# Kernel tuning notes

Measured on AMD Instinct MI355X. Metric: run time of the kernel, lower is better.

The kernel has to match this reference:

```python
import jax, jax.numpy as jnp
import numpy as np

HIDDEN = 1024
HEADS = 16
HEAD_DIM = HIDDEN // HEADS
B, S = 2, 2048


def setup_inputs() -> dict:
    key = jax.random.key(0)
    ks = jax.random.split(key, 9)
    sc = 1.0 / np.sqrt(HIDDEN)
    return {
        "hidden_state": jax.random.normal(ks[0], (B, S, HIDDEN), dtype=jnp.float32),
        "wq": jax.random.normal(ks[1], (HIDDEN, HIDDEN), dtype=jnp.float32) * sc,
        "bq": jax.random.normal(ks[2], (HIDDEN,), dtype=jnp.float32) * 0.01,
        "wk": jax.random.normal(ks[3], (HIDDEN, HIDDEN), dtype=jnp.float32) * sc,
        "bk": jax.random.normal(ks[4], (HIDDEN,), dtype=jnp.float32) * 0.01,
        "wv": jax.random.normal(ks[5], (HIDDEN, HIDDEN), dtype=jnp.float32) * sc,
        "bv": jax.random.normal(ks[6], (HIDDEN,), dtype=jnp.float32) * 0.01,
        "wo": jax.random.normal(ks[7], (HIDDEN, HIDDEN), dtype=jnp.float32) * sc,
        "bo": jax.random.normal(ks[8], (HIDDEN,), dtype=jnp.float32) * 0.01,
    }


def reference(hidden_state, wq, bq, wk, bk, wv, bv, wo, bo):
    b, s, _ = hidden_state.shape

    def split_head(x):  # [B,S,H*D] -> [B,H,S,D]
        return x.reshape(b, s, HEADS, HEAD_DIM).transpose(0, 2, 1, 3)

    q = split_head(hidden_state @ wq + bq)
    k = split_head(hidden_state @ wk + bk)
    v = split_head(hidden_state @ wv + bv)

    # NOTE: original scales by sqrt(hidden_size), NOT sqrt(head_dim)
    scale = 1.0 / jnp.sqrt(jnp.float32(HIDDEN))
    scores = jnp.einsum("bhqd,bhkd->bhqk", q, k) * scale  # [B,H,S,S]
    probs = jax.nn.softmax(scores, axis=-1)
    out = jnp.einsum("bhqk,bhkd->bhqd", probs, v)  # [B,H,S,D]

    # Faithful to source: transpose(-1,-2) then view (this is the original's
    # layout, which differs from the conventional transpose(1,2) merge)
    out = out.transpose(0, 1, 3, 2).reshape(b, -1, HEADS * HEAD_DIM)
    return out @ wo + bo
```

## Files before the change

### kernel.cpp

```cpp
#include <hip/hip_runtime.h>
#include <stdint.h>


typedef unsigned short u16;
typedef __bf16 bf16x8 __attribute__((ext_vector_type(8)));
typedef u16 u16x8 __attribute__((ext_vector_type(8)));
typedef u16 u16x4 __attribute__((ext_vector_type(4)));
typedef float f32x4 __attribute__((ext_vector_type(4)));

#define DEV static __device__ __forceinline__

DEV bf16x8 as_bf16x8(u16x8 u) { union { u16x8 u; bf16x8 b; } c; c.u = u; return c.b; }
DEV u16 f2bf(float f) {
  uint32_t u = __float_as_uint(f);
  u += 0x7fffu + ((u >> 16) & 1u);
  return (u16)(u >> 16);
}
#if __has_builtin(__builtin_amdgcn_exp2f)
DEV float ex2(float x) { return __builtin_amdgcn_exp2f(x); }
#else
DEV float ex2(float x) { return exp2f(x); }
#endif

__global__ __launch_bounds__(256) void prep_kernel(
    const float* __restrict__ hid, const float* __restrict__ w0,
    const float* __restrict__ w1, const float* __restrict__ w2,
    const float* __restrict__ w3, u16* __restrict__ Ah,
    u16* __restrict__ Wt) {
  __shared__ __align__(16) float T[64][68];
  int bid = blockIdx.x, t = threadIdx.x;
  if (bid < 2048) {
    int i = (bid * 256 + t) * 8;
    f32x4 a = *(const f32x4*)&hid[i];
    f32x4 b = *(const f32x4*)&hid[i + 4];
    u16x8 o;
#pragma unroll
    for (int j = 0; j < 4; ++j) { o[j] = f2bf(a[j]); o[j + 4] = f2bf(b[j]); }
    *(u16x8*)&Ah[i] = o;
    return;
  }
  int tb = bid - 2048;
  int z = tb >> 8, rem = tb & 255;
  const float* W = (z == 0) ? w0 : (z == 1) ? w1 : (z == 2) ? w2 : w3;
  u16* O = Wt + (size_t)z * 1024 * 1024;
  int r0 = (rem >> 4) * 64, c0 = (rem & 15) * 64;
  int i = t >> 2, js = (t & 3) * 16;
#pragma unroll
  for (int jj = 0; jj < 16; jj += 4)
    *(f32x4*)&T[i][js + jj] = *(const f32x4*)&W[(size_t)(r0 + i) * 1024 + c0 + js + jj];
  __syncthreads();
#pragma unroll
  for (int seg = 0; seg < 2; ++seg) {
    u16x8 v;
#pragma unroll
    for (int jj = 0; jj < 8; ++jj) v[jj] = f2bf(T[js + seg * 8 + jj][i]);
    *(u16x8*)&O[(size_t)(c0 + i) * 1024 + r0 + js + seg * 8] = v;
  }
}

__global__ __launch_bounds__(256, 2) void qkv_gemm(
    const u16* __restrict__ A, const u16* __restrict__ Wt,
    const float* __restrict__ bq, const float* __restrict__ bk,
    const float* __restrict__ bv, u16* __restrict__ Qb, u16* __restrict__ Kb,
    u16* __restrict__ Vt) {
  __shared__ __align__(16) u16 As[2][128 * 32], Bs[2][3][64 * 32];
  int tid = threadIdx.x, lane = tid & 63, w = tid >> 6;
  int quad = lane >> 4, l15 = lane & 15;
  int m0 = blockIdx.x * 128, n0 = blockIdx.y * 64;
  int wm = w >> 1, wn = w & 1;
  f32x4 acc[3][4][2] = {};

  const int idx0 = tid, idx1 = 256 + tid;
  const int arow0 = idx0 >> 2, ac0 = ((idx0 & 3) ^ ((arow0 >> 1) & 3)) * 8;
  const int arow1 = idx1 >> 2, ac1 = ((idx1 & 3) ^ ((arow1 >> 1) & 3)) * 8;
  const u16* Ap0 = A + (size_t)(m0 + arow0) * 1024 + ac0;
  const u16* Ap1 = A + (size_t)(m0 + arow1) * 1024 + ac1;
  const int brow = tid >> 2, bcg = ((tid & 3) ^ ((brow >> 1) & 3)) * 8;
  const u16* Bp0 = Wt + (size_t)(n0 + brow) * 1024 + bcg;
  const u16* Bp1 = Bp0 + (size_t)1024 * 1024;
  const u16* Bp2 = Bp0 + (size_t)2 * 1024 * 1024;

  u16x8 ta0, ta1, tb0, tb1, tb2;
  ta0 = *(const u16x8*)Ap0;
  ta1 = *(const u16x8*)Ap1;
  tb0 = *(const u16x8*)Bp0;
  tb1 = *(const u16x8*)Bp1;
  tb2 = *(const u16x8*)Bp2;
  *(u16x8*)&As[0][idx0 * 8] = ta0;
  *(u16x8*)&As[0][idx1 * 8] = ta1;
  *(u16x8*)&Bs[0][0][tid * 8] = tb0;
  *(u16x8*)&Bs[0][1][tid * 8] = tb1;
  *(u16x8*)&Bs[0][2][tid * 8] = tb2;
  __syncthreads();

  for (int k0 = 0; k0 < 1024; k0 += 32) {
    int cur = (k0 >> 5) & 1;
    if (k0 < 992) {
      ta0 = *(const u16x8*)(Ap0 + k0 + 32);
      ta1 = *(const u16x8*)(Ap1 + k0 + 32);
      tb0 = *(const u16x8*)(Bp0 + k0 + 32);
      tb1 = *(const u16x8*)(Bp1 + k0 + 32);
      tb2 = *(const u16x8*)(Bp2 + k0 + 32);
    }

    bf16x8 af[4];
#pragma unroll
    for (int mt = 0; mt < 4; ++mt) {
      int row = wm * 64 + mt * 16 + l15;
      af[mt] = as_bf16x8(*(const u16x8*)&As[cur][row * 32 + (quad ^ ((row >> 1) & 3)) * 8]);
    }
    __builtin_amdgcn_s_setprio(1);
#pragma unroll
    for (int z = 0; z < 3; ++z) {
      bf16x8 bfr[2];
#pragma unroll
      for (int nt = 0; nt < 2; ++nt) {
        int row = wn * 32 + nt * 16 + l15;
        bfr[nt] = as_bf16x8(*(const u16x8*)&Bs[cur][z][row * 32 + (quad ^ ((row >> 1) & 3)) * 8]);
      }
#pragma unroll
      for (int mt = 0; mt < 4; ++mt)
#pragma unroll
        for (int nt = 0; nt < 2; ++nt)
          acc[z][mt][nt] = __builtin_amdgcn_mfma_f32_16x16x32_bf16(af[mt], bfr[nt], acc[z][mt][nt], 0, 0, 0);
    }
    __builtin_amdgcn_s_setprio(0);

    if (k0 < 992) {
      int nb = cur ^ 1;
      *(u16x8*)&As[nb][idx0 * 8] = ta0;
      *(u16x8*)&As[nb][idx1 * 8] = ta1;
      *(u16x8*)&Bs[nb][0][tid * 8] = tb0;
      *(u16x8*)&Bs[nb][1][tid * 8] = tb1;
      *(u16x8*)&Bs[nb][2][tid * 8] = tb2;
    }
    __syncthreads();
  }

#pragma unroll
  for (int z = 0; z < 2; ++z) {
    const float* bias = (z == 0) ? bq : bk;
    u16* C = (z == 0) ? Qb : Kb;
    float scale = (z == 0) ? 0.045084220f : 1.0f;
#pragma unroll
    for (int nt = 0; nt < 2; ++nt) {
      int n = n0 + wn * 32 + nt * 16 + l15;
      float bb = bias[n];
      int h = n >> 6, d = n & 63;
#pragma unroll
      for (int mt = 0; mt < 4; ++mt) {
        int mbase = m0 + wm * 64 + mt * 16 + quad * 4;
#pragma unroll
        for (int r = 0; r < 4; ++r) {
          int m = mbase + r;
          int b = m >> 11, s = m & 2047;
          C[(((size_t)(b * 16 + h)) * 2048 + s) * 64 + d] =
              f2bf((acc[z][mt][nt][r] + bb) * scale);
        }
      }
    }
  }
#pragma unroll
  for (int nt = 0; nt < 2; ++nt) {
    int n = n0 + wn * 32 + nt * 16 + l15;
    float bb = bv[n];
    int h = n >> 6, d = n & 63;
#pragma unroll
    for (int mt = 0; mt < 4; ++mt) {
      int mbase = m0 + wm * 64 + mt * 16 + quad * 4;
      int b = mbase >> 11, s = mbase & 2047;
      size_t base = (((size_t)(b * 16 + h)) * 64 + d) * 2048 + s;
      u16x4 pk;
#pragma unroll
      for (int r = 0; r < 4; ++r) pk[r] = f2bf(acc[2][mt][nt][r] + bb);
      *(u16x4*)&Vt[base] = pk;
    }
  }
}

__global__ __launch_bounds__(256) void out_gemm(
    const u16* __restrict__ A, const u16* __restrict__ Wt,
    const float* __restrict__ bo, float* __restrict__ C) {
  const u16* Bt = Wt + (size_t)3 * 1024 * 1024;
  __shared__ __align__(16) u16 As[2][64 * 32], Bs[2][128 * 32];
  int tid = threadIdx.x, lane = tid & 63, w = tid >> 6;
  int quad = lane >> 4, l15 = lane & 15;
  int m0 = blockIdx.x * 64, n0 = blockIdx.y * 128;
  f32x4 acc[4][2] = {};

  const int arow = tid >> 2, acg = ((tid & 3) ^ ((arow >> 1) & 3)) * 8;
  const int bidx0 = tid, bidx1 = 256 + tid;
  const int brow0 = bidx0 >> 2, bc0 = ((bidx0 & 3) ^ ((brow0 >> 1) & 3)) * 8;
  const int brow1 = bidx1 >> 2, bc1 = ((bidx1 & 3) ^ ((brow1 >> 1) & 3)) * 8;
  const u16* Ap = A + (size_t)(m0 + arow) * 1024 + acg;
  const u16* Bp0 = Bt + (size_t)(n0 + brow0) * 1024 + bc0;
  const u16* Bp1 = Bt + (size_t)(n0 + brow1) * 1024 + bc1;

  u16x8 ta, tb0, tb1;
  ta = *(const u16x8*)Ap;
  tb0 = *(const u16x8*)Bp0;
  tb1 = *(const u16x8*)Bp1;
  *(u16x8*)&As[0][tid * 8] = ta;
  *(u16x8*)&Bs[0][bidx0 * 8] = tb0;
  *(u16x8*)&Bs[0][bidx1 * 8] = tb1;
  __syncthreads();

  for (int k0 = 0; k0 < 1024; k0 += 32) {
    int cur = (k0 >> 5) & 1;
    if (k0 < 992) {
      ta = *(const u16x8*)(Ap + k0 + 32);
      tb0 = *(const u16x8*)(Bp0 + k0 + 32);
      tb1 = *(const u16x8*)(Bp1 + k0 + 32);
    }

    bf16x8 af[4], bfr[2];
#pragma unroll
    for (int mt = 0; mt < 4; ++mt) {
      int row = mt * 16 + l15;
      af[mt] = as_bf16x8(*(const u16x8*)&As[cur][row * 32 + (quad ^ ((row >> 1) & 3)) * 8]);
    }
#pragma unroll
    for (int nt = 0; nt < 2; ++nt) {
      int row = w * 32 + nt * 16 + l15;
      bfr[nt] = as_bf16x8(*(const u16x8*)&Bs[cur][row * 32 + (quad ^ ((row >> 1) & 3)) * 8]);
    }
    __builtin_amdgcn_s_setprio(1);
#pragma unroll
    for (int mt = 0; mt < 4; ++mt)
#pragma unroll
      for (int nt = 0; nt < 2; ++nt)
        acc[mt][nt] = __builtin_amdgcn_mfma_f32_16x16x32_bf16(af[mt], bfr[nt], acc[mt][nt], 0, 0, 0);
    __builtin_amdgcn_s_setprio(0);

    if (k0 < 992) {
      int nb = cur ^ 1;
      *(u16x8*)&As[nb][tid * 8] = ta;
      *(u16x8*)&Bs[nb][bidx0 * 8] = tb0;
      *(u16x8*)&Bs[nb][bidx1 * 8] = tb1;
    }
    __syncthreads();
  }

#pragma unroll
  for (int nt = 0; nt < 2; ++nt) {
    int n = n0 + w * 32 + nt * 16 + l15;
    float bv = bo[n];
#pragma unroll
    for (int mt = 0; mt < 4; ++mt) {
      int mbase = m0 + mt * 16 + quad * 4;
#pragma unroll
      for (int r = 0; r < 4; ++r)
        C[(size_t)(mbase + r) * 1024 + n] = acc[mt][nt][r] + bv;
    }
  }
}

#define PSTR 80
__global__ __launch_bounds__(256, 2) void attn_kernel(
    const u16* __restrict__ Qb, const u16* __restrict__ Kb,
    const u16* __restrict__ Vtb, u16* __restrict__ Otb) {
  __shared__ __align__(16) u16 Ks[2][64 * PSTR], Vs[2][64 * PSTR];
  int tid = threadIdx.x, lane = tid & 63, w = tid >> 6;
  int quad = lane >> 4, l15 = lane & 15;
  int bh = blockIdx.x, q0 = blockIdx.y * 128;
  const size_t baseQK = (size_t)bh * 2048 * 64;

  bf16x8 bq[2][2];
#pragma unroll
  for (int g = 0; g < 2; ++g) {
    int qrow = q0 + w * 32 + g * 16 + l15;
#pragma unroll
    for (int ks = 0; ks < 2; ++ks)
      bq[g][ks] = as_bf16x8(*(const u16x8*)&Qb[baseQK + (size_t)qrow * 64 + (ks * 4 + quad) * 8]);
  }

  bf16x8 av1;
  {
    u16x8 o1;
#pragma unroll
    for (int j = 0; j < 8; ++j) o1[j] = 0x3F80;
    av1 = as_bf16x8(o1);
  }

  f32x4 o[2][4] = {};
  f32x4 l_acc[2] = {};
  const int km = ((l15 & 12) << 1) | (l15 & 3);
  const int srow = tid >> 3, scs = tid & 7;
  const int srow2 = 32 + srow;

  u16x8 tk[2], tv[2];
  tk[0] = *(const u16x8*)&Kb[baseQK + (size_t)srow * 64 + scs * 8];
  tk[1] = *(const u16x8*)&Kb[baseQK + (size_t)srow2 * 64 + scs * 8];
  tv[0] = *(const u16x8*)&Vtb[baseQK + (size_t)srow * 2048 + scs * 8];
  tv[1] = *(const u16x8*)&Vtb[baseQK + (size_t)srow2 * 2048 + scs * 8];
  *(u16x8*)&Ks[0][srow * PSTR + scs * 8] = tk[0];
  *(u16x8*)&Ks[0][srow2 * PSTR + scs * 8] = tk[1];
  *(u16x8*)&Vs[0][srow * PSTR + scs * 8] = tv[0];
  *(u16x8*)&Vs[0][srow2 * PSTR + scs * 8] = tv[1];
  __syncthreads();

  for (int kv = 0; kv < 32; ++kv) {
    int cur = kv & 1;
    if (kv < 31) {
      tk[0] = *(const u16x8*)&Kb[baseQK + (size_t)((kv + 1) * 64 + srow) * 64 + scs * 8];
      tk[1] = *(const u16x8*)&Kb[baseQK + (size_t)((kv + 1) * 64 + srow2) * 64 + scs * 8];
      tv[0] = *(const u16x8*)&Vtb[baseQK + (size_t)srow * 2048 + (kv + 1) * 64 + scs * 8];
      tv[1] = *(const u16x8*)&Vtb[baseQK + (size_t)srow2 * 2048 + (kv + 1) * 64 + scs * 8];
    }

    f32x4 scA[2][2] = {}, scB[2][2] = {};
    __builtin_amdgcn_s_setprio(1);
#pragma unroll
    for (int ks = 0; ks < 2; ++ks)
#pragma unroll
      for (int mtg = 0; mtg < 2; ++mtg) {
        bf16x8 akA = as_bf16x8(*(const u16x8*)&Ks[cur][(mtg * 32 + km) * PSTR + (ks * 4 + quad) * 8]);
        bf16x8 akB = as_bf16x8(*(const u16x8*)&Ks[cur][(mtg * 32 + km + 4) * PSTR + (ks * 4 + quad) * 8]);
#pragma unroll
        for (int g = 0; g < 2; ++g) {
          scA[g][mtg] = __builtin_amdgcn_mfma_f32_16x16x32_bf16(akA, bq[g][ks], scA[g][mtg], 0, 0, 0);
          scB[g][mtg] = __builtin_amdgcn_mfma_f32_16x16x32_bf16(akB, bq[g][ks], scB[g][mtg], 0, 0, 0);
        }
      }
    __builtin_amdgcn_s_setprio(0);

    bf16x8 bp[2][2];
#pragma unroll
    for (int g = 0; g < 2; ++g)
#pragma unroll
      for (int mtg = 0; mtg < 2; ++mtg) {
        float pA0 = ex2(scA[g][mtg][0]), pA1 = ex2(scA[g][mtg][1]);
        float pA2 = ex2(scA[g][mtg][2]), pA3 = ex2(scA[g][mtg][3]);
        float pB0 = ex2(scB[g][mtg][0]), pB1 = ex2(scB[g][mtg][1]);
        float pB2 = ex2(scB[g][mtg][2]), pB3 = ex2(scB[g][mtg][3]);
        bp[g][mtg] = (bf16x8){(__bf16)pA0, (__bf16)pA1, (__bf16)pA2, (__bf16)pA3,
                              (__bf16)pB0, (__bf16)pB1, (__bf16)pB2, (__bf16)pB3};
        l_acc[g] = __builtin_amdgcn_mfma_f32_16x16x32_bf16(av1, bp[g][mtg], l_acc[g], 0, 0, 0);
      }

    __builtin_amdgcn_s_setprio(1);
#pragma unroll
    for (int mtg = 0; mtg < 2; ++mtg)
#pragma unroll
      for (int dt = 0; dt < 4; ++dt) {
        bf16x8 av = as_bf16x8(*(const u16x8*)&Vs[cur][(dt * 16 + l15) * PSTR + (mtg * 4 + quad) * 8]);
#pragma unroll
        for (int g = 0; g < 2; ++g)
          o[g][dt] = __builtin_amdgcn_mfma_f32_16x16x32_bf16(av, bp[g][mtg], o[g][dt], 0, 0, 0);
      }
    __builtin_amdgcn_s_setprio(0);

    if (kv < 31) {
      int nb = cur ^ 1;
      *(u16x8*)&Ks[nb][srow * PSTR + scs * 8] = tk[0];
      *(u16x8*)&Ks[nb][srow2 * PSTR + scs * 8] = tk[1];
      *(u16x8*)&Vs[nb][srow * PSTR + scs * 8] = tv[0];
      *(u16x8*)&Vs[nb][srow2 * PSTR + scs * 8] = tv[1];
    }
    __syncthreads();
  }

#pragma unroll
  for (int g = 0; g < 2; ++g) {
    float inv = 1.0f / l_acc[g][0];
#pragma unroll
    for (int dt = 0; dt < 4; ++dt)
#pragma unroll
      for (int r = 0; r < 4; ++r) {
        int d = dt * 16 + quad * 4 + r;
        Otb[(size_t)bh * 64 * 2048 + (size_t)d * 2048 + q0 + w * 32 + g * 16 + l15] =
            f2bf(o[g][dt][r] * inv);
      }
  }
}

extern "C" void kernel_launch(void* const* d_in, const int* in_sizes, int n_in,
                              void* d_out, int out_size, void* d_ws, size_t ws_size,
                              hipStream_t stream) {
  const float* hid = (const float*)d_in[0];
  const float* wq = (const float*)d_in[1];
  const float* bq = (const float*)d_in[2];
  const float* wk = (const float*)d_in[3];
  const float* bk = (const float*)d_in[4];
  const float* wv = (const float*)d_in[5];
  const float* bv = (const float*)d_in[6];
  const float* wo = (const float*)d_in[7];
  const float* bo = (const float*)d_in[8];

  u16* ws = (u16*)d_ws;
  const size_t MB2 = (size_t)1024 * 1024;
  u16* Wt  = ws;
  u16* Ah  = ws + 4 * MB2;
  u16* Qb  = ws + 8 * MB2;
  u16* Kb  = ws + 12 * MB2;
  u16* Vtb = ws + 16 * MB2;
  u16* Otb = Ah;

  prep_kernel<<<3072, 256, 0, stream>>>(hid, wq, wk, wv, wo, Ah, Wt);
  qkv_gemm<<<dim3(32, 16), 256, 0, stream>>>(Ah, Wt, bq, bk, bv, Qb, Kb, Vtb);
  attn_kernel<<<dim3(32, 16), 256, 0, stream>>>(Qb, Kb, Vtb, Otb);
  out_gemm<<<dim3(64, 8), 256, 0, stream>>>(Otb, Wt, bo, (float*)d_out);
}
```

Before: 178.6 us.

## Split attention KV range across waves with LDS reduction of partial outputs

The attention kernel now gives each block 64 queries instead of 128 and launches twice as many blocks. Each of the four waves processes a different 32-key slice of a 128-key tile, rather than splitting queries across waves. Because softmax uses no max subtraction, the per-wave partial outputs and denominators can simply be summed with LDS atomics and then normalized. Output stores also become vectorized 16-byte writes. The intent is more parallelism and better occupancy, traded against a single-buffered tile with two barriers per iteration and an atomic reduction epilogue.

```diff
diff --git a/kernel.cpp b/kernel.cpp
--- a/kernel.cpp
+++ b/kernel.cpp
@@ -255,24 +255,30 @@
   }
 }
 
-#define PSTR 80
+#define KSTR 80
+#define VSTR 144
 __global__ __launch_bounds__(256, 2) void attn_kernel(
     const u16* __restrict__ Qb, const u16* __restrict__ Kb,
     const u16* __restrict__ Vtb, u16* __restrict__ Otb) {
-  __shared__ __align__(16) u16 Ks[2][64 * PSTR], Vs[2][64 * PSTR];
+  __shared__ __align__(16) u16 Ks[128 * KSTR];
+  __shared__ __align__(16) u16 Vs[64 * VSTR];
+  __shared__ __align__(16) float Or[64][66];
+  __shared__ float Lr[64];
   int tid = threadIdx.x, lane = tid & 63, w = tid >> 6;
   int quad = lane >> 4, l15 = lane & 15;
-  int bh = blockIdx.x, q0 = blockIdx.y * 128;
+  int bh = blockIdx.x, q0 = blockIdx.y * 64;
   const size_t baseQK = (size_t)bh * 2048 * 64;
 
-  bf16x8 bq[2][2];
-#pragma unroll
-  for (int g = 0; g < 2; ++g) {
-    int qrow = q0 + w * 32 + g * 16 + l15;
+  for (int i = tid; i < 64 * 66; i += 256) (&Or[0][0])[i] = 0.0f;
+  if (tid < 64) Lr[tid] = 0.0f;
+
+  bf16x8 bq[4][2];
+#pragma unroll
+  for (int qt = 0; qt < 4; ++qt)
 #pragma unroll
     for (int ks = 0; ks < 2; ++ks)
-      bq[g][ks] = as_bf16x8(*(const u16x8*)&Qb[baseQK + (size_t)qrow * 64 + (ks * 4 + quad) * 8]);
-  }
+      bq[qt][ks] = as_bf16x8(*(const u16x8*)&Qb[baseQK +
+          (size_t)(q0 + qt * 16 + l15) * 64 + (ks * 4 + quad) * 8]);
 
   bf16x8 av1;
   {
@@ -282,95 +288,99 @@
     av1 = as_bf16x8(o1);
   }
 
-  f32x4 o[2][4] = {};
-  f32x4 l_acc[2] = {};
+  f32x4 o[4][4] = {};
+  f32x4 l_acc[4] = {};
   const int km = ((l15 & 12) << 1) | (l15 & 3);
-  const int srow = tid >> 3, scs = tid & 7;
-  const int srow2 = 32 + srow;
-
-  u16x8 tk[2], tv[2];
-  tk[0] = *(const u16x8*)&Kb[baseQK + (size_t)srow * 64 + scs * 8];
-  tk[1] = *(const u16x8*)&Kb[baseQK + (size_t)srow2 * 64 + scs * 8];
-  tv[0] = *(const u16x8*)&Vtb[baseQK + (size_t)srow * 2048 + scs * 8];
-  tv[1] = *(const u16x8*)&Vtb[baseQK + (size_t)srow2 * 2048 + scs * 8];
-  *(u16x8*)&Ks[0][srow * PSTR + scs * 8] = tk[0];
-  *(u16x8*)&Ks[0][srow2 * PSTR + scs * 8] = tk[1];
-  *(u16x8*)&Vs[0][srow * PSTR + scs * 8] = tv[0];
-  *(u16x8*)&Vs[0][srow2 * PSTR + scs * 8] = tv[1];
+  const int kw = w * 32;
+
+  u16x8 tk[4], tv[4];
+#pragma unroll
+  for (int i = 0; i < 4; ++i) {
+    int ki = i * 256 + tid, kr = ki >> 3, kc = ki & 7;
+    tk[i] = *(const u16x8*)&Kb[baseQK + (size_t)kr * 64 + kc * 8];
+    int vd = ki >> 4, vc = ki & 15;
+    tv[i] = *(const u16x8*)&Vtb[baseQK + (size_t)vd * 2048 + vc * 8];
+  }
+
+  for (int it = 0; it < 16; ++it) {
+    __syncthreads();
+#pragma unroll
+    for (int i = 0; i < 4; ++i) {
+      int ki = i * 256 + tid, kr = ki >> 3, kc = ki & 7;
+      *(u16x8*)&Ks[kr * KSTR + kc * 8] = tk[i];
+      int vd = ki >> 4, vc = ki & 15;
+      *(u16x8*)&Vs[vd * VSTR + vc * 8] = tv[i];
+    }
+    __syncthreads();
+
+    if (it < 15) {
+#pragma unroll
+      for (int i = 0; i < 4; ++i) {
+        int ki = i * 256 + tid, kr = ki >> 3, kc = ki & 7;
+        tk[i] = *(const u16x8*)&Kb[baseQK + (size_t)((it + 1) * 128 + kr) * 64 + kc * 8];
+        int vd = ki >> 4, vc = ki & 15;
+        tv[i] = *(const u16x8*)&Vtb[baseQK + (size_t)vd * 2048 + (it + 1) * 128 + vc * 8];
+      }
+    }
+
+    bf16x8 akA[2], akB[2], av[4];
+#pragma unroll
+    for (int ks = 0; ks < 2; ++ks) {
+      akA[ks] = as_bf16x8(*(const u16x8*)&Ks[(kw + km) * KSTR + (ks * 4 + quad) * 8]);
+      akB[ks] = as_bf16x8(*(const u16x8*)&Ks[(kw + km + 4) * KSTR + (ks * 4 + quad) * 8]);
+    }
+#pragma unroll
+    for (int dt = 0; dt < 4; ++dt)
+      av[dt] = as_bf16x8(*(const u16x8*)&Vs[(dt * 16 + l15) * VSTR + kw + quad * 8]);
+
+#pragma unroll
+    for (int qt = 0; qt < 4; ++qt) {
+      f32x4 sA = {}, sB = {};
+      __builtin_amdgcn_s_setprio(1);
+      sA = __builtin_amdgcn_mfma_f32_16x16x32_bf16(akA[0], bq[qt][0], sA, 0, 0, 0);
+      sA = __builtin_amdgcn_mfma_f32_16x16x32_bf16(akA[1], bq[qt][1], sA, 0, 0, 0);
+      sB = __builtin_amdgcn_mfma_f32_16x16x32_bf16(akB[0], bq[qt][0], sB, 0, 0, 0);
+      sB = __builtin_amdgcn_mfma_f32_16x16x32_bf16(akB[1], bq[qt][1], sB, 0, 0, 0);
+      __builtin_amdgcn_s_setprio(0);
+      float pA0 = ex2(sA[0]), pA1 = ex2(sA[1]), pA2 = ex2(sA[2]), pA3 = ex2(sA[3]);
+      float pB0 = ex2(sB[0]), pB1 = ex2(sB[1]), pB2 = ex2(sB[2]), pB3 = ex2(sB[3]);
+      bf16x8 bp = (bf16x8){(__bf16)pA0, (__bf16)pA1, (__bf16)pA2, (__bf16)pA3,
+                           (__bf16)pB0, (__bf16)pB1, (__bf16)pB2, (__bf16)pB3};
+      __builtin_amdgcn_s_setprio(1);
+      l_acc[qt] = __builtin_amdgcn_mfma_f32_16x16x32_bf16(av1, bp, l_acc[qt], 0, 0, 0);
+#pragma unroll
+      for (int dt = 0; dt < 4; ++dt)
+        o[dt][qt] = __builtin_amdgcn_mfma_f32_16x16x32_bf16(av[dt], bp, o[dt][qt], 0, 0, 0);
+      __builtin_amdgcn_s_setprio(0);
+    }
+  }
+
   __syncthreads();
-
-  for (int kv = 0; kv < 32; ++kv) {
-    int cur = kv & 1;
-    if (kv < 31) {
-      tk[0] = *(const u16x8*)&Kb[baseQK + (size_t)((kv + 1) * 64 + srow) * 64 + scs * 8];
-      tk[1] = *(const u16x8*)&Kb[baseQK + (size_t)((kv + 1) * 64 + srow2) * 64 + scs * 8];
-      tv[0] = *(const u16x8*)&Vtb[baseQK + (size_t)srow * 2048 + (kv + 1) * 64 + scs * 8];
-      tv[1] = *(const u16x8*)&Vtb[baseQK + (size_t)srow2 * 2048 + (kv + 1) * 64 + scs * 8];
-    }
-
-    f32x4 scA[2][2] = {}, scB[2][2] = {};
-    __builtin_amdgcn_s_setprio(1);
-#pragma unroll
-    for (int ks = 0; ks < 2; ++ks)
-#pragma unroll
-      for (int mtg = 0; mtg < 2; ++mtg) {
-        bf16x8 akA = as_bf16x8(*(const u16x8*)&Ks[cur][(mtg * 32 + km) * PSTR + (ks * 4 + quad) * 8]);
-        bf16x8 akB = as_bf16x8(*(const u16x8*)&Ks[cur][(mtg * 32 + km + 4) * PSTR + (ks * 4 + quad) * 8]);
-#pragma unroll
-        for (int g = 0; g < 2; ++g) {
-          scA[g][mtg] = __builtin_amdgcn_mfma_f32_16x16x32_bf16(akA, bq[g][ks], scA[g][mtg], 0, 0, 0);
-          scB[g][mtg] = __builtin_amdgcn_mfma_f32_16x16x32_bf16(akB, bq[g][ks], scB[g][mtg], 0, 0, 0);
-        }
+  if (quad == 0) {
+#pragma unroll
+    for (int qt = 0; qt < 4; ++qt) atomicAdd(&Lr[qt * 16 + l15], l_acc[qt][0]);
+  }
+#pragma unroll
+  for (int dt = 0; dt < 4; ++dt)
+#pragma unroll
+    for (int qt = 0; qt < 4; ++qt)
+#pragma unroll
+      for (int r = 0; r < 4; ++r)
+        atomicAdd(&Or[qt * 16 + l15][dt * 16 + quad * 4 + r], o[dt][qt][r]);
+  __syncthreads();
+
+  {
+    int d = tid >> 2, qb4 = (tid & 3) * 16;
+#pragma unroll
+    for (int c = 0; c < 16; c += 8) {
+      u16x8 ov;
+#pragma unroll
+      for (int j = 0; j < 8; ++j) {
+        int q = qb4 + c + j;
+        ov[j] = f2bf(Or[q][d] * (1.0f / Lr[q]));
       }
-    __builtin_amdgcn_s_setprio(0);
-
-    bf16x8 bp[2][2];
-#pragma unroll
-    for (int g = 0; g < 2; ++g)
-#pragma unroll
-      for (int mtg = 0; mtg < 2; ++mtg) {
-        float pA0 = ex2(scA[g][mtg][0]), pA1 = ex2(scA[g][mtg][1]);
-        float pA2 = ex2(scA[g][mtg][2]), pA3 = ex2(scA[g][mtg][3]);
-        float pB0 = ex2(scB[g][mtg][0]), pB1 = ex2(scB[g][mtg][1]);
-        float pB2 = ex2(scB[g][mtg][2]), pB3 = ex2(scB[g][mtg][3]);
-        bp[g][mtg] = (bf16x8){(__bf16)pA0, (__bf16)pA1, (__bf16)pA2, (__bf16)pA3,
-                              (__bf16)pB0, (__bf16)pB1, (__bf16)pB2, (__bf16)pB3};
-        l_acc[g] = __builtin_amdgcn_mfma_f32_16x16x32_bf16(av1, bp[g][mtg], l_acc[g], 0, 0, 0);
-      }
-
-    __builtin_amdgcn_s_setprio(1);
-#pragma unroll
-    for (int mtg = 0; mtg < 2; ++mtg)
-#pragma unroll
-      for (int dt = 0; dt < 4; ++dt) {
-        bf16x8 av = as_bf16x8(*(const u16x8*)&Vs[cur][(dt * 16 + l15) * PSTR + (mtg * 4 + quad) * 8]);
-#pragma unroll
-        for (int g = 0; g < 2; ++g)
-          o[g][dt] = __builtin_amdgcn_mfma_f32_16x16x32_bf16(av, bp[g][mtg], o[g][dt], 0, 0, 0);
-      }
-    __builtin_amdgcn_s_setprio(0);
-
-    if (kv < 31) {
-      int nb = cur ^ 1;
-      *(u16x8*)&Ks[nb][srow * PSTR + scs * 8] = tk[0];
-      *(u16x8*)&Ks[nb][srow2 * PSTR + scs * 8] = tk[1];
-      *(u16x8*)&Vs[nb][srow * PSTR + scs * 8] = tv[0];
-      *(u16x8*)&Vs[nb][srow2 * PSTR + scs * 8] = tv[1];
-    }
-    __syncthreads();
-  }
-
-#pragma unroll
-  for (int g = 0; g < 2; ++g) {
-    float inv = 1.0f / l_acc[g][0];
-#pragma unroll
-    for (int dt = 0; dt < 4; ++dt)
-#pragma unroll
-      for (int r = 0; r < 4; ++r) {
-        int d = dt * 16 + quad * 4 + r;
-        Otb[(size_t)bh * 64 * 2048 + (size_t)d * 2048 + q0 + w * 32 + g * 16 + l15] =
-            f2bf(o[g][dt][r] * inv);
-      }
+      *(u16x8*)&Otb[baseQK + (size_t)d * 2048 + q0 + qb4 + c] = ov;
+    }
   }
 }
 
@@ -398,6 +408,6 @@
 
   prep_kernel<<<3072, 256, 0, stream>>>(hid, wq, wk, wv, wo, Ah, Wt);
   qkv_gemm<<<dim3(32, 16), 256, 0, stream>>>(Ah, Wt, bq, bk, bv, Qb, Kb, Vtb);
-  attn_kernel<<<dim3(32, 16), 256, 0, stream>>>(Qb, Kb, Vtb, Otb);
+  attn_kernel<<<dim3(32, 32), 256, 0, stream>>>(Qb, Kb, Vtb, Otb);
   out_gemm<<<dim3(64, 8), 256, 0, stream>>>(Otb, Wt, bo, (float*)d_out);
 }
```

Measured after the change: 266.9 us. 1.49x slower.
